# Kernel optimization log

Hardware: AMD Instinct MI355X
Metric: run time of the kernel (lower is better)

Reference implementation:

```python
import jax, jax.numpy as jnp
import numpy as np

B, N, C, H = 16, 800, 1024, 16
NC = 128  # cached KV length from the N==128 pass
HD = C // H


def setup_inputs() -> dict:
    key = jax.random.key(0)
    ks = jax.random.split(key, 9)
    s = 0.02  # init scale for weights
    return {
        "x": jax.random.normal(ks[0], (B, N, C), jnp.float32),
        "xpos": jax.random.normal(ks[1], (B, N, C), jnp.float32),
        "k_t": jax.random.normal(ks[2], (B, NC, C), jnp.float32),
        "v_t": jax.random.normal(ks[3], (B, NC, C), jnp.float32),
        "Wq": jax.random.normal(ks[4], (C, C), jnp.float32) * s,
        "Wk": jax.random.normal(ks[5], (C, C), jnp.float32) * s,
        "Wv": jax.random.normal(ks[6], (C, C), jnp.float32) * s,
        "Wp": jax.random.normal(ks[7], (C, C), jnp.float32) * s,
        "bp": jnp.zeros((C,), jnp.float32),
    }


def reference(x, xpos, k_t, v_t, Wq, Wk, Wv, Wp, bp):
    # N == 800 branch: q from x+xpos; k/v concat cached k_t/v_t before projection.
    b, n, c = x.shape
    scale = HD ** -0.5

    q = (x + xpos) @ Wq.T                              # [B, N, C]
    k_in = jnp.concatenate([x + xpos, k_t], axis=1)    # [B, N+NC, C]
    v_in = jnp.concatenate([x, v_t], axis=1)           # [B, N+NC, C]
    k = k_in @ Wk.T
    v = v_in @ Wv.T

    def heads(t):
        return t.reshape(b, t.shape[1], H, HD).transpose(0, 2, 1, 3)  # [B,H,L,HD]

    qh, kh, vh = heads(q), heads(k), heads(v)
    attn = jax.nn.softmax(jnp.einsum('bhqd,bhkd->bhqk', qh, kh) * scale, axis=-1)
    out = jnp.einsum('bhqk,bhkd->bhqd', attn, vh)       # [B,H,N,HD]
    out = out.transpose(0, 2, 1, 3).reshape(b, n, c)
    return out @ Wp.T + bp
```

## Files before the change

kernel.cpp:

```cpp
#include <hip/hip_runtime.h>
#include <hip/hip_bf16.h>

#define NB 16
#define NN 800
#define NCACHE 128
#define NL 928
#define CC 1024
#define NH 16
#define HD 64

typedef __attribute__((ext_vector_type(8))) short bf16x8;
typedef __attribute__((ext_vector_type(4))) float f32x4;
typedef __attribute__((ext_vector_type(2))) __bf16 bf2;

__device__ __forceinline__ short f2bf(float x) {
  union { float f; unsigned u; } c; c.f = x;
  unsigned r = c.u + 0x7fffu + ((c.u >> 16) & 1u);
  return (short)(r >> 16);
}

#define GLD_LDS(gp, lp) __builtin_amdgcn_global_load_lds( \
    (__attribute__((address_space(1))) void*)(gp),        \
    (__attribute__((address_space(3))) void*)(lp), 16, 0, 0)

#define BAR() asm volatile("s_barrier" ::: "memory")

__global__ __launch_bounds__(256) void prep_kv(
    const float* __restrict__ x, const float* __restrict__ xpos,
    const float* __restrict__ ktc, const float* __restrict__ vtc,
    short* __restrict__ k_in, short* __restrict__ v_in) {
  int idx = blockIdx.x * 256 + threadIdx.x;
  int chunk = idx & 127;
  int row = idx >> 7;
  int b = row / NL;
  int lr = row - b * NL;
  int c = chunk * 8;
  float vk[8], vv[8];
  if (lr < NN) {
    const float4* px = (const float4*)(x + ((size_t)(b * NN + lr) * CC + c));
    const float4* pp = (const float4*)(xpos + ((size_t)(b * NN + lr) * CC + c));
    float4 x0 = px[0], x1 = px[1], p0 = pp[0], p1 = pp[1];
    vv[0]=x0.x; vv[1]=x0.y; vv[2]=x0.z; vv[3]=x0.w;
    vv[4]=x1.x; vv[5]=x1.y; vv[6]=x1.z; vv[7]=x1.w;
    vk[0]=x0.x+p0.x; vk[1]=x0.y+p0.y; vk[2]=x0.z+p0.z; vk[3]=x0.w+p0.w;
    vk[4]=x1.x+p1.x; vk[5]=x1.y+p1.y; vk[6]=x1.z+p1.z; vk[7]=x1.w+p1.w;
  } else {
    const float4* pk = (const float4*)(ktc + ((size_t)(b * NCACHE + lr - NN) * CC + c));
    const float4* pv = (const float4*)(vtc + ((size_t)(b * NCACHE + lr - NN) * CC + c));
    float4 k0 = pk[0], k1 = pk[1], v0 = pv[0], v1 = pv[1];
    vk[0]=k0.x; vk[1]=k0.y; vk[2]=k0.z; vk[3]=k0.w;
    vk[4]=k1.x; vk[5]=k1.y; vk[6]=k1.z; vk[7]=k1.w;
    vv[0]=v0.x; vv[1]=v0.y; vv[2]=v0.z; vv[3]=v0.w;
    vv[4]=v1.x; vv[5]=v1.y; vv[6]=v1.z; vv[7]=v1.w;
  }
  bf16x8 ok, ov;
#pragma unroll
  for (int i = 0; i < 8; ++i) { ok[i] = f2bf(vk[i]); ov[i] = f2bf(vv[i]); }
  *(bf16x8*)(k_in + (size_t)row * CC + c) = ok;
  *(bf16x8*)(v_in + (size_t)row * CC + c) = ov;
}

__global__ __launch_bounds__(256) void prep_w(
    const float* __restrict__ Wq, const float* __restrict__ Wk,
    const float* __restrict__ Wv, const float* __restrict__ Wp,
    short* __restrict__ wout) {
  int idx = blockIdx.x * 256 + threadIdx.x;
  int wsel = idx >> 17;
  int off = (idx & 131071) * 8;
  const float* src = wsel == 0 ? Wq : wsel == 1 ? Wk : wsel == 2 ? Wv : Wp;
  float sc = wsel == 0 ? 0.18033688011112042f : 1.0f;
  const float4* p = (const float4*)(src + off);
  float4 a = p[0], b = p[1];
  bf16x8 o;
  o[0]=f2bf(a.x*sc); o[1]=f2bf(a.y*sc); o[2]=f2bf(a.z*sc); o[3]=f2bf(a.w*sc);
  o[4]=f2bf(b.x*sc); o[5]=f2bf(b.y*sc); o[6]=f2bf(b.z*sc); o[7]=f2bf(b.w*sc);
  *(bf16x8*)(wout + (size_t)wsel * 1048576 + off) = o;
}

#define READ_A8(dst, QR) \
  _Pragma("unroll") \
  for (int fr = 0; fr < 4; ++fr) \
    _Pragma("unroll") \
    for (int ks = 0; ks < 2; ++ks) \
      dst[fr][ks] = *(const bf16x8*)&lds[abase + (QR)*4096 + fr*1024 + (ks ? xk1 : xk0)];

#define READ_B8() \
  _Pragma("unroll") \
  for (int q = 0; q < 4; ++q) \
    _Pragma("unroll") \
    for (int ks = 0; ks < 2; ++ks) \
      bfv[q][ks] = *(const bf16x8*)&lds[bbase + q*1024 + (ks ? xk1 : xk0)];

#define MFMA_HALF(QR, asrc) \
  _Pragma("unroll") \
  for (int fr = 0; fr < 4; ++fr) \
    _Pragma("unroll") \
    for (int fc = 0; fc < 4; ++fc) \
      _Pragma("unroll") \
      for (int ks = 0; ks < 2; ++ks) \
        acc[(QR)*4+fr][fc] = __builtin_amdgcn_mfma_f32_16x16x32_bf16( \
            asrc[fr][ks], bfv[fc][ks], acc[(QR)*4+fr][fc], 0, 0, 0);

template<int MODE>
__global__ __launch_bounds__(512, 2) void gemm256(
    const short* __restrict__ A, const short* __restrict__ Bw,
    short* __restrict__ o0, short* __restrict__ o1,
    float* __restrict__ of, const float* __restrict__ bias) {
  __shared__ short lds[65536];
  const int tid = threadIdx.x;
  const int w = tid >> 6, l = tid & 63;
  const int wm = w >> 2, wn = w & 3;
  const int c = l & 15, g2 = l >> 4;
  const int BNT = (MODE == 2) ? 8 : 4;
  const int cpx = gridDim.x >> 3;
  const int swz = (blockIdx.x & 7) * cpx + (blockIdx.x >> 3);
  const int bm = swz / BNT, bn = swz % BNT;
  const int m0 = bm * 256, n0 = bn * 256;

  const int R0 = tid >> 3;
  const int gc0 = (tid & 7) ^ (R0 & 7);
  const short* As_ = A + (size_t)(m0 + R0) * CC + gc0 * 8;
  const short* Bs_ = Bw + (size_t)(n0 + R0) * CC + gc0 * 8;
  const int wofs = w * 512;

#define STAGE_HT(slot, src) do { \
    GLD_LDS((src), &lds[(slot) + wofs]); \
    GLD_LDS((src) + 64 * CC, &lds[(slot) + 4096 + wofs]); } while (0)

  const int xk0 = ((g2) ^ (c & 7)) * 8;
  const int xk1 = ((g2 + 4) ^ (c & 7)) * 8;

  f32x4 acc[8][4] = {};

  STAGE_HT(0,     As_);
  STAGE_HT(8192,  As_ + 128 * CC);
  STAGE_HT(16384, Bs_);
  STAGE_HT(24576, Bs_ + 128 * CC);

#pragma unroll 1
  for (int t = 0; t < 16; ++t) {
    const int pb = (t & 1) << 15;
    const int pn = pb ^ 32768;
    if (t < 15) {
      const short* as1 = As_ + (t + 1) * 64;
      const short* bs1 = Bs_ + (t + 1) * 64;
      STAGE_HT(pn,         as1);
      STAGE_HT(pn + 8192,  as1 + 128 * CC);
      STAGE_HT(pn + 16384, bs1);
      STAGE_HT(pn + 24576, bs1 + 128 * CC);
      asm volatile("s_waitcnt vmcnt(8)" ::: "memory");
    } else {
      asm volatile("s_waitcnt vmcnt(0)" ::: "memory");
    }
    BAR();
    const int abase = pb + wm * 8192 + c * 64;
    const int bbase = pb + 16384 + ((wn >> 1) << 13) + ((wn & 1) * 64 + c) * 64;
    bf16x8 afA[4][2], afB[4][2], bfv[4][2];
    READ_A8(afA, 0);
    READ_B8();
    __builtin_amdgcn_s_setprio(1);
    MFMA_HALF(0, afA);
    __builtin_amdgcn_s_setprio(0);
    READ_A8(afB, 1);
    __builtin_amdgcn_s_setprio(1);
    MFMA_HALF(1, afB);
    __builtin_amdgcn_s_setprio(0);
    BAR();
  }

#pragma unroll
  for (int fr = 0; fr < 8; ++fr)
#pragma unroll
    for (int fc = 0; fc < 4; ++fc) {
      const int row = m0 + wm * 128 + fr * 16 + g2 * 4;
      const int colw = wn * 64 + fc * 16 + c;
      if (MODE == 1) {
        const int col = n0 + colw;
        const float bv = bias[col];
#pragma unroll
        for (int j = 0; j < 4; ++j)
          of[(size_t)(row + j) * CC + col] = acc[fr][fc][j] + bv;
      } else if (MODE == 2) {
        const int col2 = n0 + colw;
        short* base = (col2 < 1024) ? o0 : o1;
        const int col = col2 & 1023;
#pragma unroll
        for (int j = 0; j < 4; ++j)
          base[(size_t)(row + j) * CC + col] = f2bf(acc[fr][fc][j]);
      } else {
        const int col = n0 + colw;
        const int b = row / NL;
        const int rb = row - b * NL;
        const int vtrow = (b * NH + (col >> 6)) * HD + (col & 63);
        ushort4 pk4;
        pk4.x = (unsigned short)f2bf(acc[fr][fc][0]);
        pk4.y = (unsigned short)f2bf(acc[fr][fc][1]);
        pk4.z = (unsigned short)f2bf(acc[fr][fc][2]);
        pk4.w = (unsigned short)f2bf(acc[fr][fc][3]);
        *(ushort4*)(o0 + (size_t)vtrow * NL + rb) = pk4;
      }
    }
}

__global__ __launch_bounds__(256, 4) void attn_fwd(
    const short* __restrict__ qb, const short* __restrict__ kbuf,
    const short* __restrict__ vtb, short* __restrict__ ob) {
  __shared__ short smem[2][4096];
  const int tid = threadIdx.x;
  const int w = tid >> 6;
  const int l = tid & 63;
  const int c = l & 15, g = l >> 4;
  const int swzb = (blockIdx.x & 7) * 224 + (blockIdx.x >> 3);
  const int bh = swzb / 7;
  const int blk7 = swzb - bh * 7;
  const int h = bh & 15, b = bh >> 4;
  const int q0 = blk7 * 128 + w * 32;
  const bool active = q0 < NN;

  const int u = l >> 3;
  const int lK = 8 * w + u;
  const int b16 = lK & 15;
  const int rpK = 8 * (b16 >> 2) + (b16 & 3) + 4 * (lK >> 4);
  const int xK = (l & 7) ^ u;
  const short* srcK = kbuf + (size_t)b * NL * CC + (size_t)rpK * CC + h * HD + xK * 8;
  const int dV = 16 * w + (l >> 2);
  const int xV = (l & 3) ^ ((l >> 3) & 3);
  const short* srcV = vtb + (size_t)bh * HD * NL + (size_t)dV * NL + xV * 8;

  bf16x8 qf[2][2];
  if (active) {
#pragma unroll
    for (int f = 0; f < 2; ++f) {
      const short* qrow = qb + ((size_t)(b * NL + q0 + f * 16 + c) * CC + h * HD + g * 8);
      qf[f][0] = *(const bf16x8*)qrow;
      qf[f][1] = *(const bf16x8*)(qrow + 32);
    }
  }

  const int koff0 = c * 64 + ((g ^ (c & 7)) << 3);
  const int koff1 = c * 64 + (((g + 4) ^ (c & 7)) << 3);
  const int voffb = 2048 + c * 32 + ((g ^ ((c >> 1) & 3)) << 3);

  f32x4 acc[2][4] = {};
  f32x4 ellv[2] = {};

  GLD_LDS(srcK, &smem[0][w * 512]);
  GLD_LDS(srcV, &smem[0][2048 + w * 512]);
  __syncthreads();

  int buf = 0;
  for (int t = 0; t < 29; ++t) {
    if (t < 28) {
      GLD_LDS(srcK + (size_t)(t + 1) * 32 * CC, &smem[buf ^ 1][w * 512]);
      GLD_LDS(srcV + (t + 1) * 32, &smem[buf ^ 1][2048 + w * 512]);
    }
    if (active) {
      const short* S = smem[buf];
      bf16x8 kd0 = *(const bf16x8*)(S + koff0);
      bf16x8 kd1 = *(const bf16x8*)(S + koff1);
      bf16x8 kd2 = *(const bf16x8*)(S + koff0 + 1024);
      bf16x8 kd3 = *(const bf16x8*)(S + koff1 + 1024);
      bf16x8 vf0 = *(const bf16x8*)(S + voffb);
      bf16x8 vf1 = *(const bf16x8*)(S + voffb + 512);
      bf16x8 vf2 = *(const bf16x8*)(S + voffb + 1024);
      bf16x8 vf3 = *(const bf16x8*)(S + voffb + 1536);
      __builtin_amdgcn_s_setprio(1);
#pragma unroll
      for (int f = 0; f < 2; ++f) {
        f32x4 z = {0.f, 0.f, 0.f, 0.f};
        f32x4 s0 = __builtin_amdgcn_mfma_f32_16x16x32_bf16(kd0, qf[f][0], z, 0, 0, 0);
        s0 = __builtin_amdgcn_mfma_f32_16x16x32_bf16(kd1, qf[f][1], s0, 0, 0, 0);
        f32x4 s1 = __builtin_amdgcn_mfma_f32_16x16x32_bf16(kd2, qf[f][0], z, 0, 0, 0);
        s1 = __builtin_amdgcn_mfma_f32_16x16x32_bf16(kd3, qf[f][1], s1, 0, 0, 0);
        f32x4 e0, e1;
        e0[0] = __builtin_amdgcn_exp2f(s0[0]);
        e0[1] = __builtin_amdgcn_exp2f(s0[1]);
        e0[2] = __builtin_amdgcn_exp2f(s0[2]);
        e0[3] = __builtin_amdgcn_exp2f(s0[3]);
        e1[0] = __builtin_amdgcn_exp2f(s1[0]);
        e1[1] = __builtin_amdgcn_exp2f(s1[1]);
        e1[2] = __builtin_amdgcn_exp2f(s1[2]);
        e1[3] = __builtin_amdgcn_exp2f(s1[3]);
        ellv[f] += e0 + e1;
        union { bf2 h2[4]; bf16x8 v; } pu;
        pu.h2[0] = bf2{(__bf16)e0[0], (__bf16)e0[1]};
        pu.h2[1] = bf2{(__bf16)e0[2], (__bf16)e0[3]};
        pu.h2[2] = bf2{(__bf16)e1[0], (__bf16)e1[1]};
        pu.h2[3] = bf2{(__bf16)e1[2], (__bf16)e1[3]};
        acc[f][0] = __builtin_amdgcn_mfma_f32_16x16x32_bf16(pu.v, vf0, acc[f][0], 0, 0, 0);
        acc[f][1] = __builtin_amdgcn_mfma_f32_16x16x32_bf16(pu.v, vf1, acc[f][1], 0, 0, 0);
        acc[f][2] = __builtin_amdgcn_mfma_f32_16x16x32_bf16(pu.v, vf2, acc[f][2], 0, 0, 0);
        acc[f][3] = __builtin_amdgcn_mfma_f32_16x16x32_bf16(pu.v, vf3, acc[f][3], 0, 0, 0);
      }
      __builtin_amdgcn_s_setprio(0);
    }
    __syncthreads();
    buf ^= 1;
  }

  if (active) {
    float rinv[2];
#pragma unroll
    for (int f = 0; f < 2; ++f) {
      float e = (ellv[f][0] + ellv[f][1]) + (ellv[f][2] + ellv[f][3]);
      e += __shfl_xor(e, 16);
      e += __shfl_xor(e, 32);
      rinv[f] = 1.0f / e;
    }
#pragma unroll
    for (int f = 0; f < 2; ++f) {
      float rj[4];
#pragma unroll
      for (int j = 0; j < 4; ++j) rj[j] = __shfl(rinv[f], g * 4 + j);
      short* orow = ob + (size_t)(b * NN + q0 + f * 16 + g * 4) * CC + h * HD + c;
#pragma unroll
      for (int n = 0; n < 4; ++n)
#pragma unroll
        for (int j = 0; j < 4; ++j)
          orow[(size_t)j * CC + n * 16] = f2bf(acc[f][n][j] * rj[j]);
    }
  }
}

extern "C" void kernel_launch(void* const* d_in, const int* in_sizes, int n_in,
                              void* d_out, int out_size, void* d_ws, size_t ws_size,
                              hipStream_t stream) {
  const float* x    = (const float*)d_in[0];
  const float* xpos = (const float*)d_in[1];
  const float* k_t  = (const float*)d_in[2];
  const float* v_t  = (const float*)d_in[3];
  const float* Wq   = (const float*)d_in[4];
  const float* Wk   = (const float*)d_in[5];
  const float* Wv   = (const float*)d_in[6];
  const float* Wp   = (const float*)d_in[7];
  const float* bp   = (const float*)d_in[8];
  float* out = (float*)d_out;

  char* ws = (char*)d_ws;
  short* k_in = (short*)ws;
  short* v_in = (short*)(ws + 30408704);
  short* wqb  = (short*)(ws + 60817408);
  short* wvb  = (short*)(ws + 65011712);
  short* wpb  = (short*)(ws + 67108864);
  short* qbuf = (short*)(ws + 69206016);
  short* kbuf = (short*)(ws + 99614720);
  short* vtb  = (short*)(ws + 130023424);
  short* attn_o = k_in;

  prep_kv<<<7424, 256, 0, stream>>>(x, xpos, k_t, v_t, k_in, v_in);
  prep_w<<<2048, 256, 0, stream>>>(Wq, Wk, Wv, Wp, wqb);
  gemm256<2><<<464, 512, 0, stream>>>(k_in, wqb, qbuf, kbuf, nullptr, nullptr);
  gemm256<3><<<232, 512, 0, stream>>>(v_in, wvb, vtb, nullptr, nullptr, nullptr);
  attn_fwd<<<1792, 256, 0, stream>>>(qbuf, kbuf, vtb, attn_o);
  gemm256<1><<<200, 512, 0, stream>>>(attn_o, wpb, nullptr, nullptr, out, bp);
}
```

Before: 248.9 us.

## Double attention KV tile to 64 keys per iteration with tail step

The attention kernel now stages 64 keys of K and V per loop iteration instead of 32. It runs 14 full iterations plus a 32-key tail, which halves the number of barriers and loop-overhead steps. The staging layout is rewritten so all 256 threads cooperatively load row-swizzled K and V tiles, and the LDS buffer doubles. The launch bound drops to 3 waves per SIMD, trading some occupancy for more work between synchronisations and higher register pressure.

```diff
diff --git a/kernel.cpp b/kernel.cpp
--- a/kernel.cpp
+++ b/kernel.cpp
@@ -202,10 +202,10 @@
     }
 }
 
-__global__ __launch_bounds__(256, 4) void attn_fwd(
+__global__ __launch_bounds__(256, 3) void attn_fwd(
     const short* __restrict__ qb, const short* __restrict__ kbuf,
     const short* __restrict__ vtb, short* __restrict__ ob) {
-  __shared__ short smem[2][4096];
+  __shared__ short smem[2][8192];
   const int tid = threadIdx.x;
   const int w = tid >> 6;
   const int l = tid & 63;
@@ -217,15 +217,14 @@
   const int q0 = blk7 * 128 + w * 32;
   const bool active = q0 < NN;
 
-  const int u = l >> 3;
-  const int lK = 8 * w + u;
-  const int b16 = lK & 15;
-  const int rpK = 8 * (b16 >> 2) + (b16 & 3) + 4 * (lK >> 4);
-  const int xK = (l & 7) ^ u;
-  const short* srcK = kbuf + (size_t)b * NL * CC + (size_t)rpK * CC + h * HD + xK * 8;
-  const int dV = 16 * w + (l >> 2);
-  const int xV = (l & 3) ^ ((l >> 3) & 3);
-  const short* srcV = vtb + (size_t)bh * HD * NL + (size_t)dV * NL + xV * 8;
+  const int r = tid >> 3, ch = tid & 7;
+  const int b16 = r & 15;
+  const int rp = 8 * (b16 >> 2) + (b16 & 3) + 4 * (r >> 4);
+  const int xch = ch ^ (r & 7);
+  const int tid8 = tid * 8;
+  const short* srcKA = kbuf + (size_t)(b * NL + rp) * CC + h * HD + xch * 8;
+  const short* srcVA = vtb + (size_t)(bh * HD + r) * NL + xch * 8;
+  const short* srcVB = vtb + (size_t)(bh * HD + 32 + r) * NL + xch * 8;
 
   bf16x8 qf[2][2];
   if (active) {
@@ -237,68 +236,121 @@
     }
   }
 
-  const int koff0 = c * 64 + ((g ^ (c & 7)) << 3);
-  const int koff1 = c * 64 + (((g + 4) ^ (c & 7)) << 3);
-  const int voffb = 2048 + c * 32 + ((g ^ ((c >> 1) & 3)) << 3);
+  int xrc[2];
+#pragma unroll
+  for (int ks = 0; ks < 2; ++ks)
+    xrc[ks] = (((ks * 4 + g) ^ (c & 7)) << 3);
 
   f32x4 acc[2][4] = {};
   f32x4 ellv[2] = {};
 
-  GLD_LDS(srcK, &smem[0][w * 512]);
-  GLD_LDS(srcV, &smem[0][2048 + w * 512]);
+  auto STG_FULL = [&](int buf, int t) {
+    GLD_LDS(srcKA + (size_t)(t * 64) * CC,      &smem[buf][tid8]);
+    GLD_LDS(srcKA + (size_t)(t * 64 + 32) * CC, &smem[buf][2048 + tid8]);
+    GLD_LDS(srcVA + t * 64,                     &smem[buf][4096 + tid8]);
+    GLD_LDS(srcVB + t * 64,                     &smem[buf][6144 + tid8]);
+  };
+  auto STG_TAIL = [&](int buf) {
+    GLD_LDS(srcKA + (size_t)896 * CC, &smem[buf][tid8]);
+    const int voff = (xch < 4) ? 896 : 864;
+    GLD_LDS(srcVA + voff, &smem[buf][4096 + tid8]);
+    GLD_LDS(srcVB + voff, &smem[buf][6144 + tid8]);
+  };
+
+  auto COMP_FULL = [&](const short* S) {
+    bf16x8 kd[4][2], vf[4][2];
+#pragma unroll
+    for (int si = 0; si < 4; ++si)
+#pragma unroll
+      for (int ks = 0; ks < 2; ++ks)
+        kd[si][ks] = *(const bf16x8*)&S[si * 1024 + c * 64 + xrc[ks]];
+#pragma unroll
+    for (int n = 0; n < 4; ++n)
+#pragma unroll
+      for (int ks = 0; ks < 2; ++ks)
+        vf[n][ks] = *(const bf16x8*)&S[4096 + (n * 16 + c) * 64 + xrc[ks]];
+    __builtin_amdgcn_s_setprio(1);
+#pragma unroll
+    for (int f = 0; f < 2; ++f) {
+      f32x4 z = {0.f, 0.f, 0.f, 0.f};
+      f32x4 s[4];
+#pragma unroll
+      for (int si = 0; si < 4; ++si) {
+        s[si] = __builtin_amdgcn_mfma_f32_16x16x32_bf16(kd[si][0], qf[f][0], z, 0, 0, 0);
+        s[si] = __builtin_amdgcn_mfma_f32_16x16x32_bf16(kd[si][1], qf[f][1], s[si], 0, 0, 0);
+      }
+      f32x4 e[4];
+#pragma unroll
+      for (int si = 0; si < 4; ++si)
+#pragma unroll
+        for (int j = 0; j < 4; ++j)
+          e[si][j] = __builtin_amdgcn_exp2f(s[si][j]);
+      ellv[f] += (e[0] + e[1]) + (e[2] + e[3]);
+      union { bf2 h2[4]; bf16x8 v; } p0, p1;
+      p0.h2[0] = bf2{(__bf16)e[0][0], (__bf16)e[0][1]};
+      p0.h2[1] = bf2{(__bf16)e[0][2], (__bf16)e[0][3]};
+      p0.h2[2] = bf2{(__bf16)e[1][0], (__bf16)e[1][1]};
+      p0.h2[3] = bf2{(__bf16)e[1][2], (__bf16)e[1][3]};
+      p1.h2[0] = bf2{(__bf16)e[2][0], (__bf16)e[2][1]};
+      p1.h2[1] = bf2{(__bf16)e[2][2], (__bf16)e[2][3]};
+      p1.h2[2] = bf2{(__bf16)e[3][0], (__bf16)e[3][1]};
+      p1.h2[3] = bf2{(__bf16)e[3][2], (__bf16)e[3][3]};
+#pragma unroll
+      for (int n = 0; n < 4; ++n) {
+        acc[f][n] = __builtin_amdgcn_mfma_f32_16x16x32_bf16(p0.v, vf[n][0], acc[f][n], 0, 0, 0);
+        acc[f][n] = __builtin_amdgcn_mfma_f32_16x16x32_bf16(p1.v, vf[n][1], acc[f][n], 0, 0, 0);
+      }
+    }
+    __builtin_amdgcn_s_setprio(0);
+  };
+
+  auto COMP_TAIL = [&](const short* S) {
+    bf16x8 kd[2][2], vf[4];
+#pragma unroll
+    for (int si = 0; si < 2; ++si)
+#pragma unroll
+      for (int ks = 0; ks < 2; ++ks)
+        kd[si][ks] = *(const bf16x8*)&S[si * 1024 + c * 64 + xrc[ks]];
+#pragma unroll
+    for (int n = 0; n < 4; ++n)
+      vf[n] = *(const bf16x8*)&S[4096 + (n * 16 + c) * 64 + xrc[0]];
+#pragma unroll
+    for (int f = 0; f < 2; ++f) {
+      f32x4 z = {0.f, 0.f, 0.f, 0.f};
+      f32x4 s[2];
+#pragma unroll
+      for (int si = 0; si < 2; ++si) {
+        s[si] = __builtin_amdgcn_mfma_f32_16x16x32_bf16(kd[si][0], qf[f][0], z, 0, 0, 0);
+        s[si] = __builtin_amdgcn_mfma_f32_16x16x32_bf16(kd[si][1], qf[f][1], s[si], 0, 0, 0);
+      }
+      f32x4 e0, e1;
+#pragma unroll
+      for (int j = 0; j < 4; ++j) { e0[j] = __builtin_amdgcn_exp2f(s[0][j]);
+                                    e1[j] = __builtin_amdgcn_exp2f(s[1][j]); }
+      ellv[f] += e0 + e1;
+      union { bf2 h2[4]; bf16x8 v; } p0;
+      p0.h2[0] = bf2{(__bf16)e0[0], (__bf16)e0[1]};
+      p0.h2[1] = bf2{(__bf16)e0[2], (__bf16)e0[3]};
+      p0.h2[2] = bf2{(__bf16)e1[0], (__bf16)e1[1]};
+      p0.h2[3] = bf2{(__bf16)e1[2], (__bf16)e1[3]};
+#pragma unroll
+      for (int n = 0; n < 4; ++n)
+        acc[f][n] = __builtin_amdgcn_mfma_f32_16x16x32_bf16(p0.v, vf[n], acc[f][n], 0, 0, 0);
+    }
+  };
+
+  STG_FULL(0, 0);
   __syncthreads();
-
   int buf = 0;
-  for (int t = 0; t < 29; ++t) {
-    if (t < 28) {
-      GLD_LDS(srcK + (size_t)(t + 1) * 32 * CC, &smem[buf ^ 1][w * 512]);
-      GLD_LDS(srcV + (t + 1) * 32, &smem[buf ^ 1][2048 + w * 512]);
-    }
-    if (active) {
-      const short* S = smem[buf];
-      bf16x8 kd0 = *(const bf16x8*)(S + koff0);
-      bf16x8 kd1 = *(const bf16x8*)(S + koff1);
-      bf16x8 kd2 = *(const bf16x8*)(S + koff0 + 1024);
-      bf16x8 kd3 = *(const bf16x8*)(S + koff1 + 1024);
-      bf16x8 vf0 = *(const bf16x8*)(S + voffb);
-      bf16x8 vf1 = *(const bf16x8*)(S + voffb + 512);
-      bf16x8 vf2 = *(const bf16x8*)(S + voffb + 1024);
-      bf16x8 vf3 = *(const bf16x8*)(S + voffb + 1536);
-      __builtin_amdgcn_s_setprio(1);
-#pragma unroll
-      for (int f = 0; f < 2; ++f) {
-        f32x4 z = {0.f, 0.f, 0.f, 0.f};
-        f32x4 s0 = __builtin_amdgcn_mfma_f32_16x16x32_bf16(kd0, qf[f][0], z, 0, 0, 0);
-        s0 = __builtin_amdgcn_mfma_f32_16x16x32_bf16(kd1, qf[f][1], s0, 0, 0, 0);
-        f32x4 s1 = __builtin_amdgcn_mfma_f32_16x16x32_bf16(kd2, qf[f][0], z, 0, 0, 0);
-        s1 = __builtin_amdgcn_mfma_f32_16x16x32_bf16(kd3, qf[f][1], s1, 0, 0, 0);
-        f32x4 e0, e1;
-        e0[0] = __builtin_amdgcn_exp2f(s0[0]);
-        e0[1] = __builtin_amdgcn_exp2f(s0[1]);
-        e0[2] = __builtin_amdgcn_exp2f(s0[2]);
-        e0[3] = __builtin_amdgcn_exp2f(s0[3]);
-        e1[0] = __builtin_amdgcn_exp2f(s1[0]);
-        e1[1] = __builtin_amdgcn_exp2f(s1[1]);
-        e1[2] = __builtin_amdgcn_exp2f(s1[2]);
-        e1[3] = __builtin_amdgcn_exp2f(s1[3]);
-        ellv[f] += e0 + e1;
-        union { bf2 h2[4]; bf16x8 v; } pu;
-        pu.h2[0] = bf2{(__bf16)e0[0], (__bf16)e0[1]};
-        pu.h2[1] = bf2{(__bf16)e0[2], (__bf16)e0[3]};
-        pu.h2[2] = bf2{(__bf16)e1[0], (__bf16)e1[1]};
-        pu.h2[3] = bf2{(__bf16)e1[2], (__bf16)e1[3]};
-        acc[f][0] = __builtin_amdgcn_mfma_f32_16x16x32_bf16(pu.v, vf0, acc[f][0], 0, 0, 0);
-        acc[f][1] = __builtin_amdgcn_mfma_f32_16x16x32_bf16(pu.v, vf1, acc[f][1], 0, 0, 0);
-        acc[f][2] = __builtin_amdgcn_mfma_f32_16x16x32_bf16(pu.v, vf2, acc[f][2], 0, 0, 0);
-        acc[f][3] = __builtin_amdgcn_mfma_f32_16x16x32_bf16(pu.v, vf3, acc[f][3], 0, 0, 0);
-      }
-      __builtin_amdgcn_s_setprio(0);
-    }
+  for (int t = 0; t < 14; ++t) {
+    if (t < 13) STG_FULL(buf ^ 1, t + 1);
+    else        STG_TAIL(buf ^ 1);
+    if (active) COMP_FULL(smem[buf]);
     __syncthreads();
     buf ^= 1;
   }
-
   if (active) {
+    COMP_TAIL(smem[buf]);
     float rinv[2];
 #pragma unroll
     for (int f = 0; f < 2; ++f) {
```

Result: no change. 247.0 us (-0.8%).
